# Kernel tuning notes

Hardware: AMD Instinct MI355X
Metric: run time of the kernel (lower is better)

Reference implementation:

```python
import jax, jax.numpy as jnp
import numpy as np

MAX_WORDS = 256  # = batch['labels'].shape[1]


def _align(hidden, word_ids, max_words):
    """Batched segment-mean: (B,S,D) subtoken states -> (B,max_words,D) word states.
    Equivalent to align_subtokens_to_words applied per sample (word_ids all valid)."""
    B, S, D = hidden.shape
    seg = (word_ids.astype(jnp.int32) + jnp.arange(B, dtype=jnp.int32)[:, None] * max_words).reshape(-1)
    sums = jax.ops.segment_sum(hidden.reshape(-1, D), seg, num_segments=B * max_words)
    cnts = jax.ops.segment_sum(jnp.ones((B * S,), hidden.dtype), seg, num_segments=B * max_words)
    out = jnp.where(cnts[:, None] > 0, sums / jnp.maximum(cnts, 1.0)[:, None], 0.0)
    return out.reshape(B, max_words, D)


def setup_inputs() -> dict:
    key = jax.random.key(0)
    ks = jax.random.split(key, 8)
    B, S, D, W = 64, 512, 768, MAX_WORDS
    h_hing_sub = jax.random.normal(ks[0], (B, S, D), dtype=jnp.float32)
    h_rob_sub = jax.random.normal(ks[1], (B, S, D), dtype=jnp.float32)
    hing_word_ids = jnp.sort(jax.random.randint(ks[2], (B, S), 0, W), axis=-1).astype(jnp.int32)
    rob_word_ids = jnp.sort(jax.random.randint(ks[3], (B, S), 0, W), axis=-1).astype(jnp.int32)
    num_words = jax.random.randint(ks[4], (B,), 1, W).astype(jnp.int32)
    router_w1 = jax.random.normal(ks[5], (2 * D, 256), dtype=jnp.float32) * (1.0 / np.sqrt(2 * D))
    router_b1 = jnp.zeros((256,), jnp.float32)
    router_w2 = jax.random.normal(ks[6], (256, 1), dtype=jnp.float32) * (1.0 / 16.0)
    router_b2 = jnp.zeros((1,), jnp.float32)
    head_w = jax.random.normal(ks[7], (D, 7), dtype=jnp.float32) * (1.0 / np.sqrt(D))
    head_b = jnp.zeros((7,), jnp.float32)
    return {
        'h_hing_sub': h_hing_sub, 'h_rob_sub': h_rob_sub,
        'hing_word_ids': hing_word_ids, 'rob_word_ids': rob_word_ids,
        'num_words': num_words,
        'router_w1': router_w1, 'router_b1': router_b1,
        'router_w2': router_w2, 'router_b2': router_b2,
        'head_w': head_w, 'head_b': head_b,
    }


def reference(h_hing_sub, h_rob_sub, hing_word_ids, rob_word_ids, num_words,
              router_w1, router_b1, router_w2, router_b2, head_w, head_b):
    W = MAX_WORDS
    # scatter-mean subtokens -> words (the dominant custom-kernel op)
    h_hing = _align(h_hing_sub, hing_word_ids, W)   # (B, W, 768)
    h_rob = _align(h_rob_sub, rob_word_ids, W)      # (B, W, 768)
    # token-level MLP router on concatenated word states (router_input='both')
    router_in = jnp.concatenate([h_hing, h_rob], axis=-1)             # (B, W, 1536)
    hdn = jax.nn.relu(jnp.einsum('bwd,dh->bwh', router_in, router_w1) + router_b1)
    alpha = jax.nn.sigmoid(jnp.einsum('bwh,ho->bwo', hdn, router_w2) + router_b2)  # (B, W, 1)
    blended = alpha * h_hing + (1.0 - alpha) * h_rob                  # (B, W, 768)
    logits = jnp.einsum('bwd,dl->bwl', blended, head_w) + head_b      # (B, W, num_labels)
    l2_disagreement = jnp.linalg.norm(h_hing - h_rob, axis=-1)        # (B, W)
    return logits, alpha.squeeze(-1), l2_disagreement
```

## Files before the change

### kernel.cpp

```cpp
#include <hip/hip_runtime.h>
#include <hip/hip_bf16.h>
#include <math.h>

#define BATCH 64
#define SEQ   512
#define DIM   768
#define NW    256
#define NT    (BATCH * NW)
#define KDIM  1536
#define HID   256
#define NL    7

#define BM  32
#define BK  64
#define BKP 72
#define NKT (KDIM / BK)

typedef __bf16 bf16_t;
typedef bf16_t bf16x4 __attribute__((ext_vector_type(4)));
typedef bf16_t bf16x8 __attribute__((ext_vector_type(8)));
typedef float  f32x4  __attribute__((ext_vector_type(4)));

__global__ __launch_bounds__(256) void convert_w1_kernel(
    const float* __restrict__ w1, bf16_t* __restrict__ w1t)
{
    __shared__ float tile[64 * 257];
    int tid = threadIdx.x;
    int kc  = blockIdx.x;

    for (int k = 0; k < 64; k++)
        tile[k * 257 + tid] = w1[(size_t)(kc * 64 + k) * HID + tid];
    __syncthreads();

    bf16_t* dst = w1t + (size_t)kc * (HID * BK);
    #pragma unroll
    for (int i = 0; i < 8; i++) {
        int ch = tid + i * 256;
        int n  = ch >> 3;
        int c  = ch & 7;
        bf16x8 v;
        #pragma unroll
        for (int j = 0; j < 8; j++)
            v[j] = (bf16_t)tile[(c * 8 + j) * 257 + n];
        *(bf16x8*)(dst + n * BK + c * 8) = v;
    }
}

__device__ __forceinline__ int lower_bound_512(const int* __restrict__ a, int v)
{
    int lo = 0, hi = SEQ;
    while (lo < hi) { int m = (lo + hi) >> 1; if (a[m] < v) lo = m + 1; else hi = m; }
    return lo;
}

__global__ __launch_bounds__(256) void align_kernel(
    const float* __restrict__ hh, const float* __restrict__ hr,
    const int* __restrict__ idh, const int* __restrict__ idr,
    bf16_t* __restrict__ X)
{
    __shared__ int rngS[16];
    int tid  = threadIdx.x;
    int lane = tid & 63;
    int wv   = tid >> 6;

    if (tid < 16) {
        int tsub  = tid >> 2;
        int which = (tid >> 1) & 1;
        int bound = tid & 1;
        int tok   = blockIdx.x * 4 + tsub;
        int b     = tok >> 8;
        int w     = tok & 255;
        const int* ids = (which ? idr : idh) + b * SEQ;
        rngS[tid] = lower_bound_512(ids, w + bound);
    }
    __syncthreads();

    int tok = blockIdx.x * 4 + wv;
    int b   = tok >> 8;
    int loH = rngS[wv * 4 + 0], hiH = rngS[wv * 4 + 1];
    int loR = rngS[wv * 4 + 2], hiR = rngS[wv * 4 + 3];

    const f32x4* baseH = (const f32x4*)(hh + (size_t)b * SEQ * DIM);
    const f32x4* baseR = (const f32x4*)(hr + (size_t)b * SEQ * DIM);

    f32x4 aH0 = {0,0,0,0}, aH1 = {0,0,0,0}, aH2 = {0,0,0,0};
    f32x4 aR0 = {0,0,0,0}, aR1 = {0,0,0,0}, aR2 = {0,0,0,0};

    for (int s = loH; s < hiH; s++) {
        const f32x4* row = baseH + (size_t)s * (DIM / 4);
        aH0 += row[lane]; aH1 += row[lane + 64]; aH2 += row[lane + 128];
    }
    for (int s = loR; s < hiR; s++) {
        const f32x4* row = baseR + (size_t)s * (DIM / 4);
        aR0 += row[lane]; aR1 += row[lane + 64]; aR2 += row[lane + 128];
    }

    float invH = (hiH > loH) ? 1.0f / (float)(hiH - loH) : 0.0f;
    float invR = (hiR > loR) ? 1.0f / (float)(hiR - loR) : 0.0f;

    bf16_t* xrow = X + (size_t)tok * KDIM;
    f32x4 accs[6] = {aH0, aH1, aH2, aR0, aR1, aR2};
    #pragma unroll
    for (int c = 0; c < 6; c++) {
        float inv = (c < 3) ? invH : invR;
        int   d0  = (c < 3) ? (lane + 64 * c) * 4 : DIM + (lane + 64 * (c - 3)) * 4;
        bf16x4 o;
        #pragma unroll
        for (int e = 0; e < 4; e++) o[e] = (bf16_t)(accs[c][e] * inv);
        *(bf16x4*)(xrow + d0) = o;
    }
}

__global__ __launch_bounds__(256) void gemm_alpha_kernel(
    const bf16_t* __restrict__ X, const bf16_t* __restrict__ w1t,
    const float* __restrict__ b1, const float* __restrict__ w2,
    const float* __restrict__ b2, float* __restrict__ out)
{
    __shared__ __align__(16) bf16_t Xs[BM][BKP];
    __shared__ __align__(16) bf16_t Ws[HID][BKP];
    __shared__ float alpha_acc[BM];

    int tid   = threadIdx.x;
    int lane  = tid & 63;
    int wv    = tid >> 6;
    int row16 = lane & 15;
    int quad  = lane >> 4;
    int tok0  = blockIdx.x * BM;

    f32x4 acc[2][4];
    #pragma unroll
    for (int mi = 0; mi < 2; mi++)
        #pragma unroll
        for (int ni = 0; ni < 4; ni++)
            acc[mi][ni] = (f32x4){0.f, 0.f, 0.f, 0.f};

    int xr = tid >> 3;
    int xc = tid & 7;

    for (int kc = 0; kc < NKT; kc++) {
        {
            const uint4* src = (const uint4*)(X + (size_t)(tok0 + xr) * KDIM + kc * BK + xc * 8);
            *(uint4*)(&Xs[xr][xc * 8]) = *src;
        }
        {
            const uint4* srcb = (const uint4*)(w1t + (size_t)kc * (HID * BK));
            #pragma unroll
            for (int i = 0; i < 8; i++) {
                int cidx = tid + i * 256;
                *(uint4*)(&Ws[cidx >> 3][(cidx & 7) * 8]) = srcb[cidx];
            }
        }
        __syncthreads();
        #pragma unroll
        for (int kk2 = 0; kk2 < 2; kk2++) {
            bf16x8 af[2], bfg[4];
            #pragma unroll
            for (int mi = 0; mi < 2; mi++)
                af[mi] = *(const bf16x8*)(&Xs[mi * 16 + row16][kk2 * 32 + quad * 8]);
            #pragma unroll
            for (int ni = 0; ni < 4; ni++)
                bfg[ni] = *(const bf16x8*)(&Ws[wv * 64 + ni * 16 + row16][kk2 * 32 + quad * 8]);
            #pragma unroll
            for (int mi = 0; mi < 2; mi++)
                #pragma unroll
                for (int ni = 0; ni < 4; ni++)
                    acc[mi][ni] = __builtin_amdgcn_mfma_f32_16x16x32_bf16(
                        af[mi], bfg[ni], acc[mi][ni], 0, 0, 0);
        }
        __syncthreads();
    }

    float w2v[4], b1v[4];
    #pragma unroll
    for (int ni = 0; ni < 4; ni++) {
        int col = wv * 64 + ni * 16 + row16;
        w2v[ni] = w2[col];
        b1v[ni] = b1[col];
    }
    if (tid < BM) alpha_acc[tid] = 0.f;
    __syncthreads();

    #pragma unroll
    for (int mi = 0; mi < 2; mi++) {
        #pragma unroll
        for (int r = 0; r < 4; r++) {
            float p = 0.f;
            #pragma unroll
            for (int ni = 0; ni < 4; ni++) {
                float v = acc[mi][ni][r] + b1v[ni];
                v = v > 0.f ? v : 0.f;
                p += v * w2v[ni];
            }
            p += __shfl_xor(p, 1);
            p += __shfl_xor(p, 2);
            p += __shfl_xor(p, 4);
            p += __shfl_xor(p, 8);
            if (row16 == 0)
                atomicAdd(&alpha_acc[mi * 16 + quad * 4 + r], p);
        }
    }
    __syncthreads();
    if (tid < BM) {
        float a = 1.f / (1.f + expf(-(alpha_acc[tid] + b2[0])));
        out[(size_t)NT * NL + tok0 + tid] = a;
    }
}

__global__ __launch_bounds__(256) void blend_kernel(
    const bf16_t* __restrict__ X, const float* __restrict__ hw,
    const float* __restrict__ hb, float* __restrict__ out)
{
    int tid  = threadIdx.x;
    int lane = tid & 63;
    int wv   = tid >> 6;
    int tok  = blockIdx.x * 4 + wv;

    const float* alpha = out + (size_t)NT * NL;
    float a = alpha[tok];
    const bf16_t* xrow = X + (size_t)tok * KDIM;

    float lg[NL] = {0.f, 0.f, 0.f, 0.f, 0.f, 0.f, 0.f};
    float l2 = 0.f;

    #pragma unroll
    for (int j = 0; j < 3; j++) {
        int d0 = (lane + 64 * j) * 4;
        bf16x4 hp = *(const bf16x4*)(xrow + d0);
        bf16x4 rp = *(const bf16x4*)(xrow + DIM + d0);
        const f32x4* hwv = (const f32x4*)(hw + (size_t)d0 * NL);
        f32x4 wv4[7];
        #pragma unroll
        for (int q = 0; q < 7; q++) wv4[q] = hwv[q];
        #pragma unroll
        for (int e = 0; e < 4; e++) {
            float hhv = (float)hp[e];
            float hrv = (float)rp[e];
            float bl  = a * hhv + (1.f - a) * hrv;
            float df  = hhv - hrv;
            l2 += df * df;
            #pragma unroll
            for (int l = 0; l < NL; l++) {
                int idx = e * NL + l;
                lg[l] += bl * wv4[idx >> 2][idx & 3];
            }
        }
    }

    #pragma unroll
    for (int off = 1; off < 64; off <<= 1) {
        #pragma unroll
        for (int l = 0; l < NL; l++) lg[l] += __shfl_xor(lg[l], off);
        l2 += __shfl_xor(l2, off);
    }

    if (lane < NL)
        out[(size_t)tok * NL + lane] = lg[lane] + hb[lane];
    else if (lane == NL)
        out[(size_t)NT * NL + NT + tok] = sqrtf(l2);
}

extern "C" void kernel_launch(void* const* d_in, const int* in_sizes, int n_in,
                              void* d_out, int out_size, void* d_ws, size_t ws_size,
                              hipStream_t stream)
{
    const float* hh  = (const float*)d_in[0];
    const float* hr  = (const float*)d_in[1];
    const int*   idh = (const int*)d_in[2];
    const int*   idr = (const int*)d_in[3];
    const float* w1  = (const float*)d_in[5];
    const float* b1  = (const float*)d_in[6];
    const float* w2  = (const float*)d_in[7];
    const float* b2  = (const float*)d_in[8];
    const float* hw  = (const float*)d_in[9];
    const float* hb  = (const float*)d_in[10];
    float* out = (float*)d_out;

    bf16_t* X   = (bf16_t*)d_ws;
    bf16_t* w1t = X + (size_t)NT * KDIM;

    convert_w1_kernel<<<NKT, 256, 0, stream>>>(w1, w1t);
    align_kernel<<<NT / 4, 256, 0, stream>>>(hh, hr, idh, idr, X);
    gemm_alpha_kernel<<<NT / BM, 256, 0, stream>>>(X, w1t, b1, w2, b2, out);
    blend_kernel<<<NT / 4, 256, 0, stream>>>(X, hw, hb, out);
}
```

Measured before the change: 297.4 us.

## Precompute word segment starts and process word chunks per wave in align

Adds a starts_kernel that binary-searches every word boundary once per (tensor, batch). Align now assigns each wave a run of 8 consecutive words of a single tensor and walks the contiguous boundaries, instead of doing per-token binary searches in shared memory. The w1 conversion becomes a smaller per-thread gather with more blocks, and the blend kernel stages head weights transposed in LDS. This adds one extra launch and per-block LDS staging in blend, and the longer per-wave loops in align may raise load imbalance.

```diff
diff --git a/kernel.cpp b/kernel.cpp
--- a/kernel.cpp
+++ b/kernel.cpp
@@ -16,6 +16,8 @@
 #define BKP 72
 #define NKT (KDIM / BK)
 
+#define WC  8
+
 typedef __bf16 bf16_t;
 typedef bf16_t bf16x4 __attribute__((ext_vector_type(4)));
 typedef bf16_t bf16x8 __attribute__((ext_vector_type(8)));
@@ -24,90 +26,83 @@
 __global__ __launch_bounds__(256) void convert_w1_kernel(
     const float* __restrict__ w1, bf16_t* __restrict__ w1t)
 {
-    __shared__ float tile[64 * 257];
-    int tid = threadIdx.x;
-    int kc  = blockIdx.x;
-
-    for (int k = 0; k < 64; k++)
-        tile[k * 257 + tid] = w1[(size_t)(kc * 64 + k) * HID + tid];
-    __syncthreads();
-
-    bf16_t* dst = w1t + (size_t)kc * (HID * BK);
-    #pragma unroll
-    for (int i = 0; i < 8; i++) {
-        int ch = tid + i * 256;
-        int n  = ch >> 3;
-        int c  = ch & 7;
-        bf16x8 v;
-        #pragma unroll
-        for (int j = 0; j < 8; j++)
-            v[j] = (bf16_t)tile[(c * 8 + j) * 257 + n];
-        *(bf16x8*)(dst + n * BK + c * 8) = v;
-    }
-}
-
-__device__ __forceinline__ int lower_bound_512(const int* __restrict__ a, int v)
-{
+    int kc = blockIdx.x >> 3;
+    int kg = blockIdx.x & 7;
+    int n  = threadIdx.x;
+    bf16x8 v;
+    #pragma unroll
+    for (int j = 0; j < 8; j++)
+        v[j] = (bf16_t)w1[(size_t)(kc * 64 + kg * 8 + j) * HID + n];
+    *(bf16x8*)(w1t + (size_t)kc * (HID * BK) + n * BK + kg * 8) = v;
+}
+
+__global__ __launch_bounds__(256) void starts_kernel(
+    const int* __restrict__ idh, const int* __restrict__ idr,
+    int* __restrict__ starts)
+{
+    int blk = blockIdx.x;
+    int t = blk >> 6;
+    int b = blk & 63;
+    const int* ids = (t ? idr : idh) + b * SEQ;
+    int w = threadIdx.x;
     int lo = 0, hi = SEQ;
-    while (lo < hi) { int m = (lo + hi) >> 1; if (a[m] < v) lo = m + 1; else hi = m; }
-    return lo;
+    while (lo < hi) {
+        int m = (lo + hi) >> 1;
+        if (ids[m] < w) lo = m + 1; else hi = m;
+    }
+    int* row = starts + blk * 257;
+    row[w] = lo;
+    if (w == 0) row[256] = SEQ;
 }
 
 __global__ __launch_bounds__(256) void align_kernel(
     const float* __restrict__ hh, const float* __restrict__ hr,
-    const int* __restrict__ idh, const int* __restrict__ idr,
-    bf16_t* __restrict__ X)
-{
-    __shared__ int rngS[16];
+    const int* __restrict__ starts, bf16_t* __restrict__ X)
+{
     int tid  = threadIdx.x;
     int lane = tid & 63;
     int wv   = tid >> 6;
-
-    if (tid < 16) {
-        int tsub  = tid >> 2;
-        int which = (tid >> 1) & 1;
-        int bound = tid & 1;
-        int tok   = blockIdx.x * 4 + tsub;
-        int b     = tok >> 8;
-        int w     = tok & 255;
-        const int* ids = (which ? idr : idh) + b * SEQ;
-        rngS[tid] = lower_bound_512(ids, w + bound);
-    }
-    __syncthreads();
-
-    int tok = blockIdx.x * 4 + wv;
-    int b   = tok >> 8;
-    int loH = rngS[wv * 4 + 0], hiH = rngS[wv * 4 + 1];
-    int loR = rngS[wv * 4 + 2], hiR = rngS[wv * 4 + 3];
-
-    const f32x4* baseH = (const f32x4*)(hh + (size_t)b * SEQ * DIM);
-    const f32x4* baseR = (const f32x4*)(hr + (size_t)b * SEQ * DIM);
-
-    f32x4 aH0 = {0,0,0,0}, aH1 = {0,0,0,0}, aH2 = {0,0,0,0};
-    f32x4 aR0 = {0,0,0,0}, aR1 = {0,0,0,0}, aR2 = {0,0,0,0};
-
-    for (int s = loH; s < hiH; s++) {
-        const f32x4* row = baseH + (size_t)s * (DIM / 4);
-        aH0 += row[lane]; aH1 += row[lane + 64]; aH2 += row[lane + 128];
-    }
-    for (int s = loR; s < hiR; s++) {
-        const f32x4* row = baseR + (size_t)s * (DIM / 4);
-        aR0 += row[lane]; aR1 += row[lane + 64]; aR2 += row[lane + 128];
-    }
-
-    float invH = (hiH > loH) ? 1.0f / (float)(hiH - loH) : 0.0f;
-    float invR = (hiR > loR) ? 1.0f / (float)(hiR - loR) : 0.0f;
-
-    bf16_t* xrow = X + (size_t)tok * KDIM;
-    f32x4 accs[6] = {aH0, aH1, aH2, aR0, aR1, aR2};
-    #pragma unroll
-    for (int c = 0; c < 6; c++) {
-        float inv = (c < 3) ? invH : invR;
-        int   d0  = (c < 3) ? (lane + 64 * c) * 4 : DIM + (lane + 64 * (c - 3)) * 4;
-        bf16x4 o;
-        #pragma unroll
-        for (int e = 0; e < 4; e++) o[e] = (bf16_t)(accs[c][e] * inv);
-        *(bf16x4*)(xrow + d0) = o;
+    int task = blockIdx.x * 4 + wv;
+    int b = task >> 6;
+    int t = (task >> 5) & 1;
+    int c = task & 31;
+    int w0 = c * WC;
+
+    const int*   st    = starts + (t * 64 + b) * 257;
+    const f32x4* base4 = (const f32x4*)((t ? hr : hh) + (size_t)b * SEQ * DIM);
+    bf16_t*      dstb  = X + (size_t)b * NW * KDIM + t * DIM;
+
+    int lo = st[w0];
+    #pragma unroll 1
+    for (int w = w0; w < w0 + WC; w++) {
+        int hi = st[w + 1];
+        bf16_t* xr = dstb + (size_t)w * KDIM;
+        if (hi > lo) {
+            f32x4 a0 = {0,0,0,0}, a1 = {0,0,0,0}, a2 = {0,0,0,0};
+            for (int s = lo; s < hi; s++) {
+                const f32x4* row = base4 + (size_t)s * (DIM / 4);
+                a0 += row[lane];
+                a1 += row[lane + 64];
+                a2 += row[lane + 128];
+            }
+            float inv = 1.0f / (float)(hi - lo);
+            bf16x4 o0, o1, o2;
+            #pragma unroll
+            for (int e = 0; e < 4; e++) {
+                o0[e] = (bf16_t)(a0[e] * inv);
+                o1[e] = (bf16_t)(a1[e] * inv);
+                o2[e] = (bf16_t)(a2[e] * inv);
+            }
+            *(bf16x4*)(xr + (lane)       * 4) = o0;
+            *(bf16x4*)(xr + (lane + 64)  * 4) = o1;
+            *(bf16x4*)(xr + (lane + 128) * 4) = o2;
+        } else {
+            bf16x4 z = {};
+            *(bf16x4*)(xr + (lane)       * 4) = z;
+            *(bf16x4*)(xr + (lane + 64)  * 4) = z;
+            *(bf16x4*)(xr + (lane + 128) * 4) = z;
+        }
+        lo = hi;
     }
 }
 
@@ -210,11 +205,18 @@
     const bf16_t* __restrict__ X, const float* __restrict__ hw,
     const float* __restrict__ hb, float* __restrict__ out)
 {
+    __shared__ float hws[NL * DIM];
     int tid  = threadIdx.x;
     int lane = tid & 63;
     int wv   = tid >> 6;
-    int tok  = blockIdx.x * 4 + wv;
-
+
+    for (int i = tid; i < DIM * NL; i += 256) {
+        int d = i / NL, l = i - d * NL;
+        hws[l * DIM + d] = hw[i];
+    }
+    __syncthreads();
+
+    int tok = blockIdx.x * 4 + wv;
     const float* alpha = out + (size_t)NT * NL;
     float a = alpha[tok];
     const bf16_t* xrow = X + (size_t)tok * KDIM;
@@ -227,22 +229,19 @@
         int d0 = (lane + 64 * j) * 4;
         bf16x4 hp = *(const bf16x4*)(xrow + d0);
         bf16x4 rp = *(const bf16x4*)(xrow + DIM + d0);
-        const f32x4* hwv = (const f32x4*)(hw + (size_t)d0 * NL);
-        f32x4 wv4[7];
-        #pragma unroll
-        for (int q = 0; q < 7; q++) wv4[q] = hwv[q];
+        float bl[4];
         #pragma unroll
         for (int e = 0; e < 4; e++) {
             float hhv = (float)hp[e];
             float hrv = (float)rp[e];
-            float bl  = a * hhv + (1.f - a) * hrv;
-            float df  = hhv - hrv;
+            bl[e] = a * hhv + (1.f - a) * hrv;
+            float df = hhv - hrv;
             l2 += df * df;
-            #pragma unroll
-            for (int l = 0; l < NL; l++) {
-                int idx = e * NL + l;
-                lg[l] += bl * wv4[idx >> 2][idx & 3];
-            }
+        }
+        #pragma unroll
+        for (int l = 0; l < NL; l++) {
+            f32x4 wv4 = *(const f32x4*)(&hws[l * DIM + d0]);
+            lg[l] += bl[0] * wv4[0] + bl[1] * wv4[1] + bl[2] * wv4[2] + bl[3] * wv4[3];
         }
     }
 
@@ -275,11 +274,13 @@
     const float* hb  = (const float*)d_in[10];
     float* out = (float*)d_out;
 
-    bf16_t* X   = (bf16_t*)d_ws;
-    bf16_t* w1t = X + (size_t)NT * KDIM;
-
-    convert_w1_kernel<<<NKT, 256, 0, stream>>>(w1, w1t);
-    align_kernel<<<NT / 4, 256, 0, stream>>>(hh, hr, idh, idr, X);
+    bf16_t* X      = (bf16_t*)d_ws;
+    bf16_t* w1t    = X + (size_t)NT * KDIM;
+    int*    starts = (int*)(w1t + (size_t)NKT * HID * BK);
+
+    convert_w1_kernel<<<192, 256, 0, stream>>>(w1, w1t);
+    starts_kernel<<<128, 256, 0, stream>>>(idh, idr, starts);
+    align_kernel<<<1024, 256, 0, stream>>>(hh, hr, starts, X);
     gemm_alpha_kernel<<<NT / BM, 256, 0, stream>>>(X, w1t, b1, w2, b2, out);
     blend_kernel<<<NT / 4, 256, 0, stream>>>(X, hw, hb, out);
 }
```

Result: slower. 305.1 us (+2.6%).
